# Kernel optimization log

Hardware: AMD Instinct MI355X
Metric: run time of the kernel (lower is better)

## Reference

```python
import jax, jax.numpy as jnp
import numpy as np

B = 4096
D = 512
N_I = 1000000
N_T = 1000000
GAMMA = 0.8
EPS = 1e-10
RHO_I = 8.0
RHO_T = 8.0
ETA_INIT = 1e-05
BETA_U = 0.5
GRAD_CLIP = 5.0
TAU_MIN, TAU_MAX = 0.005, 0.05
TAU_INIT = 0.01


def setup_inputs() -> dict:
    key = jax.random.key(0)
    k1, k2 = jax.random.split(key)
    img = jax.random.normal(k1, (B, D), jnp.float32)
    txt = jax.random.normal(k2, (B, D), jnp.float32)
    # CLIP-style L2-normalized features
    img = img / jnp.linalg.norm(img, axis=1, keepdims=True)
    txt = txt / jnp.linalg.norm(txt, axis=1, keepdims=True)
    return {
        "image_features": img,
        "text_features": txt,
        "s_I": jnp.zeros(N_I, jnp.float32),
        "s_T": jnp.zeros(N_T, jnp.float32),
        "b_I": jnp.zeros(N_I, jnp.float32),
        "b_T": jnp.zeros(N_T, jnp.float32),
        "u_I": jnp.zeros(N_I, jnp.float32),
        "u_T": jnp.zeros(N_T, jnp.float32),
        "tau_I": jnp.full((N_I,), TAU_INIT, jnp.float32),
        "tau_T": jnp.full((N_T,), TAU_INIT, jnp.float32),
        "image_ids": jnp.arange(B, dtype=jnp.int32),
        "text_ids": jnp.arange(B, dtype=jnp.int32),
        "epoch": 1,
    }


def reference(image_features, text_features, s_I, s_T, b_I, b_T, u_I, u_T,
              tau_I, tau_T, image_ids, text_ids, epoch):
    sg = jax.lax.stop_gradient
    sim = jnp.einsum('id,jd->ij', image_features, text_features)  # [B,B]
    diag = jnp.diagonal(sim)
    Bn = sim.shape[0]
    tau_img = tau_I[image_ids]  # [B]
    tau_txt = tau_T[text_ids]   # [B]
    image_diffs = sim - diag[:, None]
    text_diffs = sim - diag[None, :]
    # .detach() in the original -> stop_gradient here
    idt = sg(image_diffs / tau_img[:, None])
    tdt = sg(text_diffs / tau_txt[None, :])
    old_b_I = b_I[image_ids]
    old_b_T = b_T[text_ids]
    # running max for log-sum-exp stabilization
    b_I_row = jnp.maximum(idt.max(axis=1), old_b_I)
    b_T_col = jnp.maximum(tdt.max(axis=0), old_b_T)
    b_I_new = b_I.at[image_ids].set(b_I_row)
    b_T_new = b_T.at[text_ids].set(b_T_col)
    mask = 1.0 - jnp.eye(Bn, dtype=sim.dtype)
    exp_i = jnp.exp(idt - b_I_row[:, None]) * mask
    exp_t = jnp.exp(tdt - b_T_col[None, :]) * mask
    g_I = exp_i.sum(axis=1)
    g_T = exp_t.sum(axis=0)
    if epoch == 0:
        sI = g_I
        sT = g_T
    else:
        sI = (1.0 - GAMMA) * s_I[image_ids] * jnp.exp(old_b_I - b_I_row) + GAMMA * g_I
        sT = (1.0 - GAMMA) * s_T[text_ids] * jnp.exp(old_b_T - b_T_col) + GAMMA * g_T
    s_I_new = s_I.at[image_ids].set(sI)
    s_T_new = s_T.at[text_ids].set(sT)
    w_i = sg(exp_i / (sI[:, None] + EPS))
    w_t = sg(exp_t / (sT[None, :] + EPS))
    image_loss = (w_i * image_diffs).sum(axis=1)
    text_loss = (w_t * text_diffs).sum(axis=0)
    total_loss = image_loss.mean() + text_loss.mean()
    tw_i = jnp.log(sI / (Bn - 1)) + b_I_row + RHO_I - (w_i * idt).sum(axis=1)
    tw_t = jnp.log(sT / (Bn - 1)) + b_T_col + RHO_T - (w_t * tdt).sum(axis=0)
    # torch uses in-place clamp_ on a view, so the returned means are clipped
    tw_i = jnp.clip(tw_i, -GRAD_CLIP, GRAD_CLIP)
    tw_t = jnp.clip(tw_t, -GRAD_CLIP, GRAD_CLIP)
    u_I_val = (1.0 - BETA_U) * u_I[image_ids] + BETA_U * tw_i
    u_T_val = (1.0 - BETA_U) * u_T[text_ids] + BETA_U * tw_t
    u_I_new = u_I.at[image_ids].set(u_I_val)
    u_T_new = u_T.at[text_ids].set(u_T_val)
    tau_I_new = tau_I.at[image_ids].set(jnp.clip(tau_img - ETA_INIT * u_I_val, TAU_MIN, TAU_MAX))
    tau_T_new = tau_T.at[text_ids].set(jnp.clip(tau_txt - ETA_INIT * u_T_val, TAU_MIN, TAU_MAX))
    return (total_loss, tau_img.mean(), tau_txt.mean(), tw_i.mean(), tw_t.mean(),
            s_I_new, s_T_new, b_I_new, b_T_new, u_I_new, u_T_new, tau_I_new, tau_T_new)
```

## Files before the change

kernel.cpp:

```cpp
#include <hip/hip_runtime.h>

typedef unsigned short u16;
typedef unsigned int u32;

typedef __bf16 bf16x8 __attribute__((ext_vector_type(8)));
typedef float floatx4 __attribute__((ext_vector_type(4)));

__device__ __forceinline__ u16 f2bf(float f) {
    union { float f; u32 u; } c; c.f = f;
    u32 u = c.u;
    u32 r = u + 0x7FFFu + ((u >> 16) & 1u);
    return (u16)(r >> 16);
}
__device__ __forceinline__ float bf2f(u16 x) {
    union { u32 u; float f; } c; c.u = ((u32)x) << 16; return c.f;
}

__device__ __forceinline__ void comb(float& M, float& P0, float& P1,
                                     float m, float p0, float p1) {
    float nm = fmaxf(M, m);
    float s = __expf(M - nm), t = __expf(m - nm);
    P0 = P0 * s + p0 * t;
    P1 = P1 * s + p1 * t;
    M = nm;
}

__device__ __forceinline__ void gload16(const void* g, void* l) {
    __builtin_amdgcn_global_load_lds(
        (const __attribute__((address_space(1))) void*)g,
        (__attribute__((address_space(3))) void*)l, 16, 0, 0);
}

__global__ __launch_bounds__(256) void presplit(
    const float* __restrict__ a, const float* __restrict__ b,
    u16* __restrict__ Ah, u16* __restrict__ Al,
    u16* __restrict__ Bh, u16* __restrict__ Bl, int n,
    const float* __restrict__ tauI, const float* __restrict__ tauT,
    const int* __restrict__ img_ids, const int* __restrict__ txt_ids,
    float* __restrict__ taur, float* __restrict__ tauc) {
    if (blockIdx.y == 0 && blockIdx.x < 16) {
        int t = blockIdx.x * 256 + threadIdx.x;
        taur[t] = tauI[img_ids[t]];
        tauc[t] = tauT[txt_ids[t]];
    }
    const float* src = blockIdx.y ? b : a;
    u16* dh = blockIdx.y ? Bh : Ah;
    u16* dl = blockIdx.y ? Bl : Al;
    int i = (blockIdx.x * 256 + threadIdx.x) * 8;
    if (i >= n) return;
    float4 v0 = *(const float4*)&src[i];
    float4 v1 = *(const float4*)&src[i + 4];
    float xs[8] = {v0.x, v0.y, v0.z, v0.w, v1.x, v1.y, v1.z, v1.w};
    u16 h[8], l[8];
#pragma unroll
    for (int e = 0; e < 8; e++) {
        h[e] = f2bf(xs[e]);
        l[e] = f2bf(xs[e] - bf2f(h[e]));
    }
    int r = i >> 9, k = i & 511;
    int off = (((r >> 4) << 4) + (k >> 5)) * 512 + ((((k >> 3) & 3) << 4) + (r & 15)) * 8;
    *(uint4*)&dh[off] = *(uint4*)h;
    *(uint4*)&dl[off] = *(uint4*)l;
}

__global__ __launch_bounds__(256, 2) void gemm_flash(
    const u16* __restrict__ Ah, const u16* __restrict__ Al,
    const u16* __restrict__ Bh, const u16* __restrict__ Bl,
    const float* __restrict__ taur, const float* __restrict__ tauc,
    float* __restrict__ rowpart, float* __restrict__ colpart,
    float* __restrict__ diag,
    const float* __restrict__ p0, const float* __restrict__ p1,
    const float* __restrict__ p2, const float* __restrict__ p3,
    const float* __restrict__ p4, const float* __restrict__ p5,
    const float* __restrict__ p6, const float* __restrict__ p7,
    float* __restrict__ out, long long n) {
    __shared__ u16 tiles[32768];
    __shared__ float redbuf[1536];

    const int bid  = blockIdx.x;
    const int tid  = threadIdx.x;
    const int wave = tid >> 6, lane = tid & 63;
    const int lr = lane & 15, quad = lane >> 4;
    const int waveM = wave >> 1, waveN = wave & 1;
    const int x = bid & 7, s = bid >> 3;
    const int rowtile = (x >> 2) * 16 + (s >> 3);
    const int coltile = (x & 3) * 8 + (s & 7);
    const int rowBase = rowtile * 128;
    const int colBase = coltile * 128;

    const u16* gb = (wave == 0) ? Ah : (wave == 1) ? Al : (wave == 2) ? Bh : Bl;
    const int sbase = (wave < 2) ? rowBase : colBase;

#define STAGE(slice, bufb)                                                    \
    {                                                                         \
        _Pragma("unroll")                                                     \
        for (int j = 0; j < 8; j++) {                                         \
            size_t ge = ((size_t)(sbase + j * 16 + (slice))) * 512 + lane * 8;\
            gload16(gb + ge, &tiles[(bufb) + (wave * 8 + j) * 512]);          \
        }                                                                     \
    }

    floatx4 acc[4][4];
#pragma unroll
    for (int mi = 0; mi < 4; mi++)
#pragma unroll
        for (int ni = 0; ni < 4; ni++) acc[mi][ni] = (floatx4)0.0f;

    const int Gq = (int)((n - 3) >> 2);
    float* dst5 = out + 5;

    STAGE(0, 0)

    if (bid == 0 && tid < 32) {
        int arr = tid >> 2, j = tid & 3;
        const float* sp = (arr & 4) ? ((arr & 2) ? ((arr & 1) ? p7 : p6) : ((arr & 1) ? p5 : p4))
                                    : ((arr & 2) ? ((arr & 1) ? p3 : p2) : ((arr & 1) ? p1 : p0));
        float* dp = dst5 + (size_t)arr * (size_t)n;
        long long tail0 = 3 + 4 * (long long)Gq;
        if (j < 3) dp[j] = sp[j];
        else
            for (long long z = tail0; z < n; z++) dp[z] = sp[z];
    }
    __syncthreads();

#pragma unroll 1
    for (int t = 0; t < 16; t++) {
        const int cb = (t & 1) << 14;
        const int nb = cb ^ 16384;
        if (t < 15) STAGE(t + 1, nb)

        bool docopy = false;
        float c0 = 0.f, c1 = 0.f, c2 = 0.f, c3 = 0.f;
        int ck = 0; long long ce = 0;
        if (t < 8) {
            int c = bid * 256 + tid + t * 262144;
            ck = c >> 18;
            int g = c & 262143;
            if (g < Gq) {
                docopy = true;
                ce = 3 + 4 * (long long)g;
                const float* sp = (ck & 4) ? ((ck & 2) ? ((ck & 1) ? p7 : p6) : ((ck & 1) ? p5 : p4))
                                           : ((ck & 2) ? ((ck & 1) ? p3 : p2) : ((ck & 1) ? p1 : p0));
                c0 = sp[ce]; c1 = sp[ce + 1]; c2 = sp[ce + 2]; c3 = sp[ce + 3];
            }
        }

        {
            const int ab = cb + lane * 8;
            bf16x8 afh[4], afl[4], bfh[4], bfl[4];
#pragma unroll
            for (int mi = 0; mi < 4; mi++) {
                afh[mi] = *(const bf16x8*)&tiles[ab + (waveM * 4 + mi) * 512];
                afl[mi] = *(const bf16x8*)&tiles[ab + (8 + waveM * 4 + mi) * 512];
            }
#pragma unroll
            for (int ni = 0; ni < 4; ni++) {
                bfh[ni] = *(const bf16x8*)&tiles[ab + (16 + waveN * 4 + ni) * 512];
                bfl[ni] = *(const bf16x8*)&tiles[ab + (24 + waveN * 4 + ni) * 512];
            }
#pragma unroll
            for (int mi = 0; mi < 4; mi++)
#pragma unroll
                for (int ni = 0; ni < 4; ni++) {
                    acc[mi][ni] = __builtin_amdgcn_mfma_f32_16x16x32_bf16(afh[mi], bfh[ni], acc[mi][ni], 0, 0, 0);
                    acc[mi][ni] = __builtin_amdgcn_mfma_f32_16x16x32_bf16(afh[mi], bfl[ni], acc[mi][ni], 0, 0, 0);
                    acc[mi][ni] = __builtin_amdgcn_mfma_f32_16x16x32_bf16(afl[mi], bfh[ni], acc[mi][ni], 0, 0, 0);
                }
        }

        if (docopy) {
            float4 q = {c0, c1, c2, c3};
            *(float4*)&dst5[(size_t)ck * (size_t)n + ce] = q;
        }
        __syncthreads();
    }
#undef STAGE


    if (rowtile == coltile && waveM == waveN) {
#pragma unroll
        for (int mi = 0; mi < 4; mi++)
#pragma unroll
            for (int r = 0; r < 4; r++)
                if (lr == quad * 4 + r)
                    diag[colBase + waveN * 64 + mi * 16 + lr] = acc[mi][mi][r];
    }

#pragma unroll
    for (int mi = 0; mi < 4; mi++) {
#pragma unroll
        for (int r = 0; r < 4; r++) {
            int row_local = waveM * 64 + mi * 16 + quad * 4 + r;
            float vmax = fmaxf(fmaxf(acc[mi][0][r], acc[mi][1][r]),
                               fmaxf(acc[mi][2][r], acc[mi][3][r]));
#pragma unroll
            for (int mask = 1; mask <= 8; mask <<= 1)
                vmax = fmaxf(vmax, __shfl_xor(vmax, mask));
            float it = 1.0f / taur[rowBase + row_local];
            float M = vmax * it;
            float P0 = 0.f, P1 = 0.f;
#pragma unroll
            for (int ni = 0; ni < 4; ni++) {
                float y = acc[mi][ni][r] * it;
                float e = __expf(y - M);
                P0 += e;
                P1 += y * e;
            }
#pragma unroll
            for (int mask = 1; mask <= 8; mask <<= 1) {
                P0 += __shfl_xor(P0, mask);
                P1 += __shfl_xor(P1, mask);
            }
            if (lr == 0) {
                int xx = (row_local * 2 + waveN) * 3;
                redbuf[xx] = M; redbuf[xx + 1] = P0; redbuf[xx + 2] = P1;
            }
        }
    }

#pragma unroll
    for (int ni = 0; ni < 4; ni++) {
        int col_local = waveN * 64 + ni * 16 + lr;
        float vmax = -3.4e38f;
#pragma unroll
        for (int mi = 0; mi < 4; mi++)
            vmax = fmaxf(vmax,
                fmaxf(fmaxf(acc[mi][ni][0], acc[mi][ni][1]),
                      fmaxf(acc[mi][ni][2], acc[mi][ni][3])));
#pragma unroll
        for (int mask = 16; mask <= 32; mask <<= 1)
            vmax = fmaxf(vmax, __shfl_xor(vmax, mask));
        float it = 1.0f / tauc[colBase + col_local];
        float M = vmax * it;
        float P0 = 0.f, P1 = 0.f;
#pragma unroll
        for (int mi = 0; mi < 4; mi++)
#pragma unroll
            for (int r = 0; r < 4; r++) {
                float y = acc[mi][ni][r] * it;
                float e = __expf(y - M);
                P0 += e;
                P1 += y * e;
            }
#pragma unroll
        for (int mask = 16; mask <= 32; mask <<= 1) {
            P0 += __shfl_xor(P0, mask);
            P1 += __shfl_xor(P1, mask);
        }
        if (quad == 0) {
            int xx = 768 + (col_local * 2 + waveM) * 3;
            redbuf[xx] = M; redbuf[xx + 1] = P0; redbuf[xx + 2] = P1;
        }
    }
    __syncthreads();

    if (tid < 128) {
        int xx = tid * 6;
        float M = redbuf[xx], P0 = redbuf[xx + 1], P1 = redbuf[xx + 2];
        comb(M, P0, P1, redbuf[xx + 3], redbuf[xx + 4], redbuf[xx + 5]);
        float* dst = &rowpart[(size_t)(rowBase + tid) * 96 + coltile * 3];
        dst[0] = M; dst[1] = P0; dst[2] = P1;
    } else {
        int c = tid - 128;
        int xx = 768 + c * 6;
        float M = redbuf[xx], P0 = redbuf[xx + 1], P1 = redbuf[xx + 2];
        comb(M, P0, P1, redbuf[xx + 3], redbuf[xx + 4], redbuf[xx + 5]);
        float* dst = &colpart[(size_t)(colBase + c) * 96 + rowtile * 3];
        dst[0] = M; dst[1] = P0; dst[2] = P1;
    }
}

struct FinArgs {
    const float* rowpart; const float* colpart; const float* diag;
    const float* tauI; const float* sI; const float* bI; const float* uI;
    const float* tauT; const float* sT; const float* bT; const float* uT;
    const int* img_ids; const int* txt_ids; const int* epoch_p;
    float* out; float* rowbuf; long long n;
};

__global__ __launch_bounds__(256) void rows_final(FinArgs a) {
    int t = blockIdx.x * 256 + threadIdx.x;
    int side = t >> 12, i = t & 4095;
    const float* part   = side ? a.colpart : a.rowpart;
    const int*   ids    = side ? a.txt_ids : a.img_ids;
    const float* tau_in = side ? a.tauT : a.tauI;
    const float* s_in   = side ? a.sT   : a.sI;
    const float* b_in   = side ? a.bT   : a.bI;
    const float* u_in   = side ? a.uT   : a.uI;

    const int id = ids[i];
    const float dg = a.diag[i];

    const float4* p4 = (const float4*)(part + (size_t)i * 96);
    float v[96];
#pragma unroll
    for (int k = 0; k < 24; k++) {
        float4 q = p4[k];
        v[4 * k]     = q.x;
        v[4 * k + 1] = q.y;
        v[4 * k + 2] = q.z;
        v[4 * k + 3] = q.w;
    }
    float M = -3.4e38f, P0 = 0.f, P1 = 0.f;
#pragma unroll
    for (int k = 0; k < 32; k++)
        comb(M, P0, P1, v[3 * k], v[3 * k + 1], v[3 * k + 2]);

    const float tau   = tau_in[id];
    const float old_b = b_in[id];
    const float old_s = s_in[id];
    const float old_u = u_in[id];
    const float y_ii  = dg / tau;

    float b_row = fmaxf(M - y_ii, old_b);
    float e  = expf(M - y_ii - b_row);
    float S0 = P0 * e - expf(-b_row);
    float S1 = (P1 - y_ii * P0) * e;

    float g = S0;
    float sI = (*a.epoch_p == 0) ? g
             : 0.2f * old_s * expf(old_b - b_row) + 0.8f * g;
    float denom = sI + 1e-10f;
    float wsum = S1 / denom;
    float lossr = tau * wsum;
    float tw = logf(sI * (1.0f / 4095.0f)) + b_row + 8.0f - wsum;
    tw = fminf(fmaxf(tw, -5.0f), 5.0f);
    float uval = 0.5f * old_u + 0.5f * tw;
    float taun = fminf(fmaxf(tau - 1e-5f * uval, 0.005f), 0.05f);

    float* sect = a.out + 5;
    sect[(size_t)(0 + side) * (size_t)a.n + id] = sI;
    sect[(size_t)(2 + side) * (size_t)a.n + id] = b_row;
    sect[(size_t)(4 + side) * (size_t)a.n + id] = uval;
    sect[(size_t)(6 + side) * (size_t)a.n + id] = taun;

    a.rowbuf[(2 * side + 0) * 4096 + i] = lossr;
    a.rowbuf[(2 * side + 1) * 4096 + i] = tw;
}

__global__ __launch_bounds__(256) void scalars(
    const float* __restrict__ rows,
    const float* __restrict__ tau_I, const float* __restrict__ tau_T,
    const int* __restrict__ image_ids, const int* __restrict__ text_ids,
    float* __restrict__ out) {
    int tid = threadIdx.x;
    int lane = tid & 63, wv = tid >> 6;
    float a[6] = {0, 0, 0, 0, 0, 0};
    for (int e = tid; e < 4096; e += 256) {
        a[0] += rows[0 * 4096 + e];
        a[1] += rows[1 * 4096 + e];
        a[2] += rows[2 * 4096 + e];
        a[3] += rows[3 * 4096 + e];
        a[4] += tau_I[image_ids[e]];
        a[5] += tau_T[text_ids[e]];
    }
    __shared__ float sred[4][6];
#pragma unroll
    for (int k = 0; k < 6; k++)
        for (int o = 32; o > 0; o >>= 1) a[k] += __shfl_xor(a[k], o);
    if (lane == 0)
#pragma unroll
        for (int k = 0; k < 6; k++) sred[wv][k] = a[k];
    __syncthreads();
    if (tid == 0) {
#pragma unroll
        for (int k = 0; k < 6; k++)
            a[k] = sred[0][k] + sred[1][k] + sred[2][k] + sred[3][k];
        const float inv = 1.0f / 4096.0f;
        out[0] = (a[0] + a[2]) * inv;
        out[1] = a[4] * inv;
        out[2] = a[5] * inv;
        out[3] = a[1] * inv;
        out[4] = a[3] * inv;
    }
}

extern "C" void kernel_launch(void* const* d_in, const int* in_sizes, int n_in,
                              void* d_out, int out_size, void* d_ws, size_t ws_size,
                              hipStream_t stream) {
    const float* img   = (const float*)d_in[0];
    const float* txt   = (const float*)d_in[1];
    const float* s_I   = (const float*)d_in[2];
    const float* s_T   = (const float*)d_in[3];
    const float* b_I   = (const float*)d_in[4];
    const float* b_T   = (const float*)d_in[5];
    const float* u_I   = (const float*)d_in[6];
    const float* u_T   = (const float*)d_in[7];
    const float* tau_I = (const float*)d_in[8];
    const float* tau_T = (const float*)d_in[9];
    const int* image_ids = (const int*)d_in[10];
    const int* text_ids  = (const int*)d_in[11];
    const int* epoch     = (const int*)d_in[12];
    float* out = (float*)d_out;
    const long long n = in_sizes[2];
    const int nfeat = in_sizes[0];

    const size_t MB = 1024 * 1024;
    u16* Ah = (u16*)d_ws;
    u16* Al = Ah + (size_t)nfeat;
    u16* Bh = Al + (size_t)nfeat;
    u16* Bl = Bh + (size_t)nfeat;
    float* rowpart = (float*)((char*)d_ws + 16 * MB);
    float* colpart = (float*)((char*)d_ws + 18 * MB);
    float* diag    = (float*)((char*)d_ws + 20 * MB);
    float* taur    = (float*)((char*)d_ws + 20 * MB + 256 * 1024);
    float* tauc    = (float*)((char*)d_ws + 20 * MB + 512 * 1024);
    float* rows    = (float*)((char*)d_ws + 21 * MB);

    presplit<<<dim3((nfeat / 8 + 255) / 256, 2), 256, 0, stream>>>(
        img, txt, Ah, Al, Bh, Bl, nfeat,
        tau_I, tau_T, image_ids, text_ids, taur, tauc);

    gemm_flash<<<1024, 256, 0, stream>>>(
        Ah, Al, Bh, Bl, taur, tauc, rowpart, colpart, diag,
        s_I, s_T, b_I, b_T, u_I, u_T, tau_I, tau_T, out, n);

    FinArgs fa;
    fa.rowpart = rowpart; fa.colpart = colpart; fa.diag = diag;
    fa.tauI = tau_I; fa.sI = s_I; fa.bI = b_I; fa.uI = u_I;
    fa.tauT = tau_T; fa.sT = s_T; fa.bT = b_T; fa.uT = u_T;
    fa.img_ids = image_ids; fa.txt_ids = text_ids; fa.epoch_p = epoch;
    fa.out = out; fa.rowbuf = rows; fa.n = n;
    rows_final<<<32, 256, 0, stream>>>(fa);

    scalars<<<1, 256, 0, stream>>>(rows, tau_I, tau_T, image_ids, text_ids, out);
}
```

Baseline: 192.9 us.

## Enlarge GEMM block tile to 256x256 with 8 waves per block

Switches the fused split-bf16 GEMM from 128x128 tiles with 4 waves to 256x256 tiles with 8 waves (512 threads), so each wave computes 128x64 of the output. Shared memory doubles and the reduction buffer now reuses the tile storage. The partial-stat arrays shrink from 32 to 16 partials per row/column, and the finishing kernel is updated to match. This improves operand reuse and halves the partial traffic, at the cost of only 256 blocks on 256 CUs (one wave of blocks) and higher register pressure from 32 accumulators per wave.

Result: slower. 329.2 us (+70.7%).

```diff
diff --git a/kernel.cpp b/kernel.cpp
--- a/kernel.cpp
+++ b/kernel.cpp
@@ -63,7 +63,7 @@
     *(uint4*)&dl[off] = *(uint4*)l;
 }
 
-__global__ __launch_bounds__(256, 2) void gemm_flash(
+__global__ __launch_bounds__(512, 2) void gemm_flash(
     const u16* __restrict__ Ah, const u16* __restrict__ Al,
     const u16* __restrict__ Bh, const u16* __restrict__ Bl,
     const float* __restrict__ taur, const float* __restrict__ tauc,
@@ -74,35 +74,37 @@
     const float* __restrict__ p4, const float* __restrict__ p5,
     const float* __restrict__ p6, const float* __restrict__ p7,
     float* __restrict__ out, long long n) {
-    __shared__ u16 tiles[32768];
-    __shared__ float redbuf[1536];
+    __shared__ u16 tiles[65536];
 
     const int bid  = blockIdx.x;
     const int tid  = threadIdx.x;
     const int wave = tid >> 6, lane = tid & 63;
     const int lr = lane & 15, quad = lane >> 4;
-    const int waveM = wave >> 1, waveN = wave & 1;
+    const int waveM = wave >> 2, waveN = wave & 3;
     const int x = bid & 7, s = bid >> 3;
-    const int rowtile = (x >> 2) * 16 + (s >> 3);
-    const int coltile = (x & 3) * 8 + (s & 7);
-    const int rowBase = rowtile * 128;
-    const int colBase = coltile * 128;
-
-    const u16* gb = (wave == 0) ? Ah : (wave == 1) ? Al : (wave == 2) ? Bh : Bl;
-    const int sbase = (wave < 2) ? rowBase : colBase;
+    const int rowtile = (x >> 2) * 8 + (s >> 2);
+    const int coltile = (x & 3) * 4 + (s & 3);
+    const int rowBase = rowtile * 256;
+    const int colBase = coltile * 256;
+
+    const int sa = wave >> 1;
+    const u16* gb = (sa == 0) ? Ah : (sa == 1) ? Al : (sa == 2) ? Bh : Bl;
+    const int base16 = ((sa < 2) ? rowBase : colBase) >> 4;
+    const int jb = (wave & 1) * 8;
 
 #define STAGE(slice, bufb)                                                    \
     {                                                                         \
         _Pragma("unroll")                                                     \
         for (int j = 0; j < 8; j++) {                                         \
-            size_t ge = ((size_t)(sbase + j * 16 + (slice))) * 512 + lane * 8;\
+            size_t ge = ((size_t)(base16 + jb + j)) * 8192 +                  \
+                        (size_t)(slice) * 512 + lane * 8;                     \
             gload16(gb + ge, &tiles[(bufb) + (wave * 8 + j) * 512]);          \
         }                                                                     \
     }
 
-    floatx4 acc[4][4];
-#pragma unroll
-    for (int mi = 0; mi < 4; mi++)
+    floatx4 acc[8][4];
+#pragma unroll
+    for (int mi = 0; mi < 8; mi++)
 #pragma unroll
         for (int ni = 0; ni < 4; ni++) acc[mi][ni] = (floatx4)0.0f;
 
@@ -125,15 +127,15 @@
 
 #pragma unroll 1
     for (int t = 0; t < 16; t++) {
-        const int cb = (t & 1) << 14;
-        const int nb = cb ^ 16384;
+        const int cb = (t & 1) << 15;
+        const int nb = cb ^ 32768;
         if (t < 15) STAGE(t + 1, nb)
 
         bool docopy = false;
         float c0 = 0.f, c1 = 0.f, c2 = 0.f, c3 = 0.f;
         int ck = 0; long long ce = 0;
-        if (t < 8) {
-            int c = bid * 256 + tid + t * 262144;
+        {
+            int c = bid * 512 + tid + t * 131072;
             ck = c >> 18;
             int g = c & 262143;
             if (g < Gq) {
@@ -147,25 +149,23 @@
 
         {
             const int ab = cb + lane * 8;
-            bf16x8 afh[4], afl[4], bfh[4], bfl[4];
-#pragma unroll
-            for (int mi = 0; mi < 4; mi++) {
-                afh[mi] = *(const bf16x8*)&tiles[ab + (waveM * 4 + mi) * 512];
-                afl[mi] = *(const bf16x8*)&tiles[ab + (8 + waveM * 4 + mi) * 512];
-            }
+            bf16x8 bh[4], bl[4];
 #pragma unroll
             for (int ni = 0; ni < 4; ni++) {
-                bfh[ni] = *(const bf16x8*)&tiles[ab + (16 + waveN * 4 + ni) * 512];
-                bfl[ni] = *(const bf16x8*)&tiles[ab + (24 + waveN * 4 + ni) * 512];
-            }
-#pragma unroll
-            for (int mi = 0; mi < 4; mi++)
+                bh[ni] = *(const bf16x8*)&tiles[ab + (32 + waveN * 4 + ni) * 512];
+                bl[ni] = *(const bf16x8*)&tiles[ab + (48 + waveN * 4 + ni) * 512];
+            }
+#pragma unroll
+            for (int mi = 0; mi < 8; mi++) {
+                bf16x8 ah = *(const bf16x8*)&tiles[ab + (waveM * 8 + mi) * 512];
+                bf16x8 al = *(const bf16x8*)&tiles[ab + (16 + waveM * 8 + mi) * 512];
 #pragma unroll
                 for (int ni = 0; ni < 4; ni++) {
-                    acc[mi][ni] = __builtin_amdgcn_mfma_f32_16x16x32_bf16(afh[mi], bfh[ni], acc[mi][ni], 0, 0, 0);
-                    acc[mi][ni] = __builtin_amdgcn_mfma_f32_16x16x32_bf16(afh[mi], bfl[ni], acc[mi][ni], 0, 0, 0);
-                    acc[mi][ni] = __builtin_amdgcn_mfma_f32_16x16x32_bf16(afl[mi], bfh[ni], acc[mi][ni], 0, 0, 0);
+                    acc[mi][ni] = __builtin_amdgcn_mfma_f32_16x16x32_bf16(ah, bh[ni], acc[mi][ni], 0, 0, 0);
+                    acc[mi][ni] = __builtin_amdgcn_mfma_f32_16x16x32_bf16(ah, bl[ni], acc[mi][ni], 0, 0, 0);
+                    acc[mi][ni] = __builtin_amdgcn_mfma_f32_16x16x32_bf16(al, bh[ni], acc[mi][ni], 0, 0, 0);
                 }
+            }
         }
 
         if (docopy) {
@@ -176,21 +176,24 @@
     }
 #undef STAGE
 
-
-    if (rowtile == coltile && waveM == waveN) {
-#pragma unroll
-        for (int mi = 0; mi < 4; mi++)
+    float* redbuf = (float*)tiles;
+
+    if (rowtile == coltile && (waveN >> 1) == waveM) {
+#pragma unroll
+        for (int ni = 0; ni < 4; ni++) {
+            int mi = (waveN & 1) * 4 + ni;
 #pragma unroll
             for (int r = 0; r < 4; r++)
                 if (lr == quad * 4 + r)
-                    diag[colBase + waveN * 64 + mi * 16 + lr] = acc[mi][mi][r];
-    }
-
-#pragma unroll
-    for (int mi = 0; mi < 4; mi++) {
+                    diag[colBase + waveN * 64 + ni * 16 + lr] = acc[mi][ni][r];
+        }
+    }
+
+#pragma unroll
+    for (int mi = 0; mi < 8; mi++) {
 #pragma unroll
         for (int r = 0; r < 4; r++) {
-            int row_local = waveM * 64 + mi * 16 + quad * 4 + r;
+            int row_local = waveM * 128 + mi * 16 + quad * 4 + r;
             float vmax = fmaxf(fmaxf(acc[mi][0][r], acc[mi][1][r]),
                                fmaxf(acc[mi][2][r], acc[mi][3][r]));
 #pragma unroll
@@ -212,7 +215,7 @@
                 P1 += __shfl_xor(P1, mask);
             }
             if (lr == 0) {
-                int xx = (row_local * 2 + waveN) * 3;
+                int xx = (row_local * 4 + waveN) * 3;
                 redbuf[xx] = M; redbuf[xx + 1] = P0; redbuf[xx + 2] = P1;
             }
         }
@@ -223,7 +226,7 @@
         int col_local = waveN * 64 + ni * 16 + lr;
         float vmax = -3.4e38f;
 #pragma unroll
-        for (int mi = 0; mi < 4; mi++)
+        for (int mi = 0; mi < 8; mi++)
             vmax = fmaxf(vmax,
                 fmaxf(fmaxf(acc[mi][ni][0], acc[mi][ni][1]),
                       fmaxf(acc[mi][ni][2], acc[mi][ni][3])));
@@ -234,7 +237,7 @@
         float M = vmax * it;
         float P0 = 0.f, P1 = 0.f;
 #pragma unroll
-        for (int mi = 0; mi < 4; mi++)
+        for (int mi = 0; mi < 8; mi++)
 #pragma unroll
             for (int r = 0; r < 4; r++) {
                 float y = acc[mi][ni][r] * it;
@@ -248,24 +251,26 @@
             P1 += __shfl_xor(P1, mask);
         }
         if (quad == 0) {
-            int xx = 768 + (col_local * 2 + waveM) * 3;
+            int xx = 3072 + (col_local * 2 + waveM) * 3;
             redbuf[xx] = M; redbuf[xx + 1] = P0; redbuf[xx + 2] = P1;
         }
     }
     __syncthreads();
 
-    if (tid < 128) {
-        int xx = tid * 6;
+    if (tid < 256) {
+        int xx = tid * 12;
         float M = redbuf[xx], P0 = redbuf[xx + 1], P1 = redbuf[xx + 2];
         comb(M, P0, P1, redbuf[xx + 3], redbuf[xx + 4], redbuf[xx + 5]);
-        float* dst = &rowpart[(size_t)(rowBase + tid) * 96 + coltile * 3];
+        comb(M, P0, P1, redbuf[xx + 6], redbuf[xx + 7], redbuf[xx + 8]);
+        comb(M, P0, P1, redbuf[xx + 9], redbuf[xx + 10], redbuf[xx + 11]);
+        float* dst = &rowpart[(size_t)(rowBase + tid) * 48 + coltile * 3];
         dst[0] = M; dst[1] = P0; dst[2] = P1;
     } else {
-        int c = tid - 128;
-        int xx = 768 + c * 6;
+        int c = tid - 256;
+        int xx = 3072 + c * 6;
         float M = redbuf[xx], P0 = redbuf[xx + 1], P1 = redbuf[xx + 2];
         comb(M, P0, P1, redbuf[xx + 3], redbuf[xx + 4], redbuf[xx + 5]);
-        float* dst = &colpart[(size_t)(colBase + c) * 96 + rowtile * 3];
+        float* dst = &colpart[(size_t)(colBase + c) * 48 + rowtile * 3];
         dst[0] = M; dst[1] = P0; dst[2] = P1;
     }
 }
@@ -291,10 +296,10 @@
     const int id = ids[i];
     const float dg = a.diag[i];
 
-    const float4* p4 = (const float4*)(part + (size_t)i * 96);
-    float v[96];
-#pragma unroll
-    for (int k = 0; k < 24; k++) {
+    const float4* p4 = (const float4*)(part + (size_t)i * 48);
+    float v[48];
+#pragma unroll
+    for (int k = 0; k < 12; k++) {
         float4 q = p4[k];
         v[4 * k]     = q.x;
         v[4 * k + 1] = q.y;
@@ -303,7 +308,7 @@
     }
     float M = -3.4e38f, P0 = 0.f, P1 = 0.f;
 #pragma unroll
-    for (int k = 0; k < 32; k++)
+    for (int k = 0; k < 16; k++)
         comb(M, P0, P1, v[3 * k], v[3 * k + 1], v[3 * k + 2]);
 
     const float tau   = tau_in[id];
@@ -411,7 +416,7 @@
         img, txt, Ah, Al, Bh, Bl, nfeat,
         tau_I, tau_T, image_ids, text_ids, taur, tauc);
 
-    gemm_flash<<<1024, 256, 0, stream>>>(
+    gemm_flash<<<256, 512, 0, stream>>>(
         Ah, Al, Bh, Bl, taur, tauc, rowpart, colpart, diag,
         s_I, s_T, b_I, b_T, u_I, u_T, tau_I, tau_T, out, n);
 
```
